# Performance work log

Hardware: AMD Instinct MI355X
Metric: run time of the kernel (lower is better)

Reference implementation:

```python
import jax, jax.numpy as jnp
import numpy as np

B, C, H, W = 8, 16, 512, 512


def setup_inputs() -> dict:
    key = jax.random.key(0)
    k1, k2 = jax.random.split(key)
    src = jax.random.normal(k1, (B, C, H, W), dtype=jnp.float32)
    flow = jax.random.normal(k2, (B, 2, H, W), dtype=jnp.float32)
    return {"src": src, "flow": flow}


def _warp(src, flow):
    b, c, h, w = src.shape
    # identity grid: channel 0 = row index (y), channel 1 = col index (x)
    gy, gx = jnp.meshgrid(jnp.arange(h, dtype=jnp.float32),
                          jnp.arange(w, dtype=jnp.float32), indexing='ij')
    new_y = gy[None, :, :] + flow[:, 0]   # [B,H,W]
    new_x = gx[None, :, :] + flow[:, 1]   # [B,H,W]
    # normalize to [-1,1] (as the torch module does) ...
    ny = 2.0 * (new_y / (h - 1) - 0.5)
    nx = 2.0 * (new_x / (w - 1) - 0.5)
    # ... then un-normalize as grid_sample(align_corners=True) does
    py = (ny + 1.0) * 0.5 * (h - 1)
    px = (nx + 1.0) * 0.5 * (w - 1)
    # padding_mode='border': clip source coords before computing weights
    py = jnp.clip(py, 0.0, h - 1)
    px = jnp.clip(px, 0.0, w - 1)
    y0f = jnp.floor(py)
    x0f = jnp.floor(px)
    wy = (py - y0f)[:, None, :, :]   # [B,1,H,W]
    wx = (px - x0f)[:, None, :, :]
    y0 = jnp.clip(y0f.astype(jnp.int32), 0, h - 1)
    x0 = jnp.clip(x0f.astype(jnp.int32), 0, w - 1)
    y1 = jnp.clip(y0 + 1, 0, h - 1)
    x1 = jnp.clip(x0 + 1, 0, w - 1)

    def gather(s, yi, xi):
        return s[:, yi, xi]  # [C,H,W]

    g = jax.vmap(gather)
    v00 = g(src, y0, x0)
    v01 = g(src, y0, x1)
    v10 = g(src, y1, x0)
    v11 = g(src, y1, x1)
    return (v00 * (1.0 - wy) * (1.0 - wx)
            + v01 * (1.0 - wy) * wx
            + v10 * wy * (1.0 - wx)
            + v11 * wy * wx)


def reference(src, flow):
    return _warp(src, flow)
```

## Files before the change

kernel.cpp:

```cpp
#include <hip/hip_runtime.h>


#define BB 8
#define CC 16
#define HH 512
#define WW 512

typedef float f2u __attribute__((ext_vector_type(2), aligned(4)));

__global__ __launch_bounds__(256) void warp_kernel(
    const float* __restrict__ src,
    const float* __restrict__ flow,
    float* __restrict__ out)
{
    const int HW = HH * WW;
    const int NWG = (BB * HW) / 256;
    const int CHUNK = NWG / 8;

    int bid = (int)blockIdx.x;
    int swz = (bid & 7) * CHUNK + (bid >> 3);
    int idx = swz * 256 + (int)threadIdx.x;

    int b  = idx >> 18;
    int hw = idx & (HW - 1);
    int h  = hw >> 9;
    int w  = hw & (WW - 1);

    const float* fb = flow + (size_t)b * 2 * HW;
    float f0 = __builtin_nontemporal_load(fb + hw);
    float f1 = __builtin_nontemporal_load(fb + HW + hw);

    float py = fminf(fmaxf((float)h + f0, 0.0f), (float)(HH - 1));
    float px = fminf(fmaxf((float)w + f1, 0.0f), (float)(WW - 1));

    int yl = min((int)py, HH - 2);
    int xl = min((int)px, WW - 2);
    float wy = py - (float)yl;
    float wx = px - (float)xl;

    float w00 = (1.0f - wy) * (1.0f - wx);
    float w01 = (1.0f - wy) * wx;
    float w10 = wy * (1.0f - wx);
    float w11 = wy * wx;

    int u0 = yl * WW + xl;
    int u1 = u0 + WW;

    const float* sb = src + (size_t)b * CC * HW;
    float*       ob = out + (size_t)b * CC * HW;

    #pragma unroll
    for (int c = 0; c < CC; ++c) {
        const float* sc = sb + c * HW;
        f2u r0 = *reinterpret_cast<const f2u*>(sc + u0);
        f2u r1 = *reinterpret_cast<const f2u*>(sc + u1);
        float v = r0.x * w00 + r0.y * w01
                + r1.x * w10 + r1.y * w11;
        __builtin_nontemporal_store(v, ob + c * HW + hw);
    }
}

extern "C" void kernel_launch(void* const* d_in, const int* in_sizes, int n_in,
                              void* d_out, int out_size, void* d_ws, size_t ws_size,
                              hipStream_t stream) {
    const float* src  = (const float*)d_in[0];
    const float* flow = (const float*)d_in[1];
    float* out = (float*)d_out;

    const int n_pix = BB * HH * WW;
    dim3 block(256);
    dim3 grid(n_pix / 256);
    warp_kernel<<<grid, block, 0, stream>>>(src, flow, out);
}
```

Measured before the change: 292.2 us.

## Stage source row band in LDS per block and gather bilinear taps from shared memory

Each block now handles two output rows (1024 pixels, four per thread). It finds the range of source rows those pixels touch with a wave and block min/max reduction, then copies up to 16 source rows per channel into LDS with coalesced 16-byte loads. The bilinear taps are read from LDS, and pixels outside the staged band fall back to direct global gathers. This replaces scattered global gathers with coalesced streaming, at the cost of extra barriers per channel, a larger LDS footprint and possibly redundant row loads when the touched band is small.

```diff
diff --git a/kernel.cpp b/kernel.cpp
--- a/kernel.cpp
+++ b/kernel.cpp
@@ -5,58 +5,115 @@
 #define CC 16
 #define HH 512
 #define WW 512
+#define HW (HH*WW)
+
+#define NR_MAX  16
+#define LSTRIDE 516
 
 typedef float f2u __attribute__((ext_vector_type(2), aligned(4)));
+typedef float f4u __attribute__((ext_vector_type(4), aligned(16)));
 
 __global__ __launch_bounds__(256) void warp_kernel(
     const float* __restrict__ src,
     const float* __restrict__ flow,
     float* __restrict__ out)
 {
-    const int HW = HH * WW;
-    const int NWG = (BB * HW) / 256;
-    const int CHUNK = NWG / 8;
+    __shared__ float tile[NR_MAX * LSTRIDE];
+    __shared__ int redmn[4], redmx[4];
 
     int bid = (int)blockIdx.x;
-    int swz = (bid & 7) * CHUNK + (bid >> 3);
-    int idx = swz * 256 + (int)threadIdx.x;
-
-    int b  = idx >> 18;
-    int hw = idx & (HW - 1);
-    int h  = hw >> 9;
-    int w  = hw & (WW - 1);
+    int swz = (bid & 7) * 256 + (bid >> 3);
+    int b   = swz >> 8;
+    int rp  = swz & 255;
+    int hw0 = rp << 10;
+    int t   = (int)threadIdx.x;
 
     const float* fb = flow + (size_t)b * 2 * HW;
-    float f0 = __builtin_nontemporal_load(fb + hw);
-    float f1 = __builtin_nontemporal_load(fb + HW + hw);
 
-    float py = fminf(fmaxf((float)h + f0, 0.0f), (float)(HH - 1));
-    float px = fminf(fmaxf((float)w + f1, 0.0f), (float)(WW - 1));
+    int   yl[4], xl[4], loff[4], inw[4];
+    float W00[4], W01[4], W10[4], W11[4];
 
-    int yl = min((int)py, HH - 2);
-    int xl = min((int)px, WW - 2);
-    float wy = py - (float)yl;
-    float wx = px - (float)xl;
+    #pragma unroll
+    for (int p = 0; p < 4; ++p) {
+        int hw = hw0 + t + (p << 8);
+        int h = hw >> 9, w = hw & (WW - 1);
+        float f0 = __builtin_nontemporal_load(fb + hw);
+        float f1 = __builtin_nontemporal_load(fb + HW + hw);
+        float py = fminf(fmaxf((float)h + f0, 0.0f), (float)(HH - 1));
+        float px = fminf(fmaxf((float)w + f1, 0.0f), (float)(WW - 1));
+        int y = min((int)py, HH - 2);
+        int x = min((int)px, WW - 2);
+        float wy = py - (float)y, wx = px - (float)x;
+        yl[p] = y; xl[p] = x;
+        W00[p] = (1.0f - wy) * (1.0f - wx);
+        W01[p] = (1.0f - wy) * wx;
+        W10[p] = wy * (1.0f - wx);
+        W11[p] = wy * wx;
+    }
 
-    float w00 = (1.0f - wy) * (1.0f - wx);
-    float w01 = (1.0f - wy) * wx;
-    float w10 = wy * (1.0f - wx);
-    float w11 = wy * wx;
+    int mn = min(min(yl[0], yl[1]), min(yl[2], yl[3]));
+    int mx = max(max(yl[0], yl[1]), max(yl[2], yl[3]));
+    #pragma unroll
+    for (int off = 32; off; off >>= 1) {
+        mn = min(mn, __shfl_xor(mn, off));
+        mx = max(mx, __shfl_xor(mx, off));
+    }
+    int wid = t >> 6;
+    if ((t & 63) == 0) { redmn[wid] = mn; redmx[wid] = mx; }
+    __syncthreads();
+    int ys = min(min(redmn[0], redmn[1]), min(redmn[2], redmn[3]));
+    int ye = max(max(redmx[0], redmx[1]), max(redmx[2], redmx[3]));
+    int nrows = min(ye + 2 - ys, NR_MAX);
+    int ntot  = nrows << 9;
 
-    int u0 = yl * WW + xl;
-    int u1 = u0 + WW;
+    #pragma unroll
+    for (int p = 0; p < 4; ++p) {
+        loff[p] = (yl[p] - ys) * LSTRIDE + xl[p];
+        inw[p]  = (yl[p] - ys) <= (nrows - 2);
+    }
 
     const float* sb = src + (size_t)b * CC * HW;
     float*       ob = out + (size_t)b * CC * HW;
+    int t4 = t << 2;
 
-    #pragma unroll
+    const float* sc = sb + (ys << 9);
+    const float* sg = sb;
+    float*       oc = ob;
+
     for (int c = 0; c < CC; ++c) {
-        const float* sc = sb + c * HW;
-        f2u r0 = *reinterpret_cast<const f2u*>(sc + u0);
-        f2u r1 = *reinterpret_cast<const f2u*>(sc + u1);
-        float v = r0.x * w00 + r0.y * w01
-                + r1.x * w10 + r1.y * w11;
-        __builtin_nontemporal_store(v, ob + c * HW + hw);
+        f4u sr[8];
+        #pragma unroll
+        for (int k = 0; k < 8; ++k) {
+            int i = t4 + (k << 10);
+            if (i < ntot) sr[k] = *reinterpret_cast<const f4u*>(sc + i);
+        }
+        if (c) __syncthreads();
+        #pragma unroll
+        for (int k = 0; k < 8; ++k) {
+            int i = t4 + (k << 10);
+            if (i < ntot) {
+                int r = i >> 9, cl = i & (WW - 1);
+                *reinterpret_cast<f4u*>(&tile[r * LSTRIDE + cl]) = sr[k];
+            }
+        }
+        __syncthreads();
+
+        #pragma unroll
+        for (int p = 0; p < 4; ++p) {
+            float v;
+            if (inw[p]) {
+                f2u a = *reinterpret_cast<const f2u*>(&tile[loff[p]]);
+                f2u d = *reinterpret_cast<const f2u*>(&tile[loff[p] + LSTRIDE]);
+                v = a.x * W00[p] + a.y * W01[p] + d.x * W10[p] + d.y * W11[p];
+            } else {
+                int u0 = (yl[p] << 9) + xl[p];
+                f2u a = *reinterpret_cast<const f2u*>(sg + u0);
+                f2u d = *reinterpret_cast<const f2u*>(sg + u0 + WW);
+                v = a.x * W00[p] + a.y * W01[p] + d.x * W10[p] + d.y * W11[p];
+            }
+            __builtin_nontemporal_store(v, oc + hw0 + t + (p << 8));
+        }
+        sc += HW; sg += HW; oc += HW;
     }
 }
 
@@ -67,8 +124,7 @@
     const float* flow = (const float*)d_in[1];
     float* out = (float*)d_out;
 
-    const int n_pix = BB * HH * WW;
     dim3 block(256);
-    dim3 grid(n_pix / 256);
+    dim3 grid(BB * (HH / 2));
     warp_kernel<<<grid, block, 0, stream>>>(src, flow, out);
 }
```

Result: slower. 374.5 us (+28.2%).
